# Performance work log

Measured on AMD Instinct MI355X. Metric: run time of the kernel, lower is better.

The kernel has to match this reference:

```python
import jax, jax.numpy as jnp
import numpy as np

B, N, D_NET = 16, 2048, 64
L_SFC, D_VNF = 16, 32
HID, NHEAD, DFF, NLAYERS = 128, 4, 8, 2
NUM_NODES = 1024
SEQ = L_SFC + 2
EPS = 1e-5


def setup_inputs() -> dict:
    key = jax.random.key(0)
    ks = iter(jax.random.split(key, 40))
    def nrm(shape, scale=0.02):
        return (jax.random.normal(next(ks), shape, dtype=jnp.float32) * scale)
    inp = {
        'net_state': jax.random.normal(next(ks), (B, N, D_NET), dtype=jnp.float32),
        'sfc_state': jax.random.normal(next(ks), (B, L_SFC, D_VNF), dtype=jnp.float32),
        'node_pair': jax.random.randint(next(ks), (B, 2), 0, NUM_NODES),
        # manual attention projections (torch Linear layout [out,in])
        'Wq': nrm((4 * D_NET, D_NET)), 'bq': jnp.zeros((4 * D_NET,), jnp.float32),
        'Wk': nrm((4 * D_NET, D_NET)), 'bk': jnp.zeros((4 * D_NET,), jnp.float32),
        'Wv': nrm((4 * D_NET, D_NET)), 'bv': jnp.zeros((4 * D_NET,), jnp.float32),
        'net_W': nrm((HID, 4 * D_NET)), 'net_b': jnp.zeros((HID,), jnp.float32),
        'node_embed': nrm((NUM_NODES, D_VNF), 1.0),
        'sfc_W': nrm((HID, D_VNF)), 'sfc_b': jnp.zeros((HID,), jnp.float32),
        'pos_embed': nrm((SEQ, HID), 1.0),
        # 2 TransformerEncoderLayers, stacked on leading axis
        'qkv_w': nrm((NLAYERS, 3 * HID, HID)), 'qkv_b': jnp.zeros((NLAYERS, 3 * HID), jnp.float32),
        'out_w': nrm((NLAYERS, HID, HID)), 'out_b': jnp.zeros((NLAYERS, HID), jnp.float32),
        'ln1_w': jnp.ones((NLAYERS, HID), jnp.float32), 'ln1_b': jnp.zeros((NLAYERS, HID), jnp.float32),
        'lin1_w': nrm((NLAYERS, DFF, HID)), 'lin1_b': jnp.zeros((NLAYERS, DFF), jnp.float32),
        'lin2_w': nrm((NLAYERS, HID, DFF)), 'lin2_b': jnp.zeros((NLAYERS, HID), jnp.float32),
        'ln2_w': jnp.ones((NLAYERS, HID), jnp.float32), 'ln2_b': jnp.zeros((NLAYERS, HID), jnp.float32),
    }
    return inp


def _layernorm(x, w, b):
    mu = jnp.mean(x, axis=-1, keepdims=True)
    var = jnp.mean(jnp.square(x - mu), axis=-1, keepdims=True)
    return (x - mu) * jax.lax.rsqrt(var + EPS) * w + b


def _mha(x, w_qkv, b_qkv, w_out, b_out, pad_mask):
    Bx, S, H = x.shape
    hd = H // NHEAD
    qkv = x @ w_qkv.T + b_qkv                      # [B,S,3H]
    q, k, v = jnp.split(qkv, 3, axis=-1)
    q = q.reshape(Bx, S, NHEAD, hd).transpose(0, 2, 1, 3)
    k = k.reshape(Bx, S, NHEAD, hd).transpose(0, 2, 1, 3)
    v = v.reshape(Bx, S, NHEAD, hd).transpose(0, 2, 1, 3)
    scores = jnp.einsum('bhqd,bhkd->bhqk', q, k) / jnp.float32(hd) ** 0.5
    scores = scores + jnp.where(pad_mask[:, None, None, :], -1e9, 0.0)
    attn = jax.nn.softmax(scores, axis=-1)
    o = jnp.einsum('bhqk,bhkd->bhqd', attn, v).transpose(0, 2, 1, 3).reshape(Bx, S, H)
    return o @ w_out.T + b_out


def reference(net_state, sfc_state, node_pair, Wq, bq, Wk, bk, Wv, bv,
              net_W, net_b, node_embed, sfc_W, sfc_b, pos_embed,
              qkv_w, qkv_b, out_w, out_b, ln1_w, ln1_b,
              lin1_w, lin1_b, lin2_w, lin2_b, ln2_w, ln2_b):
    # --- net branch: manual single-head self-attention over nodes ---
    Q = net_state @ Wq.T + bq                       # [B,N,4D]
    K = net_state @ Wk.T + bk
    V = net_state @ Wv.T + bv
    scores = jnp.einsum('bnd,bmd->bnm', Q, K) / jnp.float32(net_state.shape[-1]) ** 0.5
    net_out = jax.nn.softmax(scores, axis=-1) @ V   # [B,N,4D]
    net_out = net_out @ net_W.T + net_b             # [B,N,HID]
    # --- sfc branch ---
    pair_emb = node_embed[node_pair]                # [B,2,D_VNF]
    sfc = jnp.concatenate([pair_emb[:, :1], sfc_state, pair_emb[:, 1:2]], axis=1)
    pad_mask = jnp.sum(jnp.abs(sfc), axis=-1) == 0  # [B,SEQ]
    x = sfc @ sfc_W.T + sfc_b + pos_embed[None, :sfc.shape[1]]
    for l in range(NLAYERS):  # post-norm TransformerEncoderLayer, relu, dropout=0
        x = _layernorm(x + _mha(x, qkv_w[l], qkv_b[l], out_w[l], out_b[l], pad_mask), ln1_w[l], ln1_b[l])
        ff = jax.nn.relu(x @ lin1_w[l].T + lin1_b[l]) @ lin2_w[l].T + lin2_b[l]
        x = _layernorm(x + ff, ln2_w[l], ln2_b[l])
    return jnp.concatenate([net_out, x], axis=1)    # [B, N+SEQ, HID]
```

## Files before the change

### kernel.cpp

```cpp
#include <hip/hip_runtime.h>
#include <cstdint>
#include <cstddef>

#define B_   16
#define N_   2048
#define DN   64
#define DQ   256
#define HID_ 128
#define SEQ_ 18
#define OUTR 2066
#define KVB  32

typedef __attribute__((ext_vector_type(4)))  float f32x4;
typedef __attribute__((ext_vector_type(16))) float f32x16;
typedef __attribute__((ext_vector_type(8)))  short bf16x8;

__device__ __forceinline__ unsigned cvtpk(float lo, float hi) {
  unsigned w;
  asm("v_cvt_pk_bf16_f32 %0, %1, %2" : "=v"(w) : "v"(lo), "v"(hi));
  return w;
}
__device__ __forceinline__ short f2bf(float f) {
  union { float f; unsigned u; } v; v.f = f;
  unsigned r = v.u + 0x7fffu + ((v.u >> 16) & 1u);
  return (short)(r >> 16);
}
__device__ __forceinline__ bf16x8 cvt8(const float* p) {
  f32x4 a = *(const f32x4*)p, b = *(const f32x4*)(p + 4);
  union { unsigned u[4]; bf16x8 v; } r;
  r.u[0] = cvtpk(a[0], a[1]); r.u[1] = cvtpk(a[2], a[3]);
  r.u[2] = cvtpk(b[0], b[1]); r.u[3] = cvtpk(b[2], b[3]);
  return r.v;
}
__device__ __forceinline__ float hadd4(f32x4 v) { return (v[0] + v[1]) + (v[2] + v[3]); }

__device__ __forceinline__ bf16x8 mkfrag(unsigned wa, unsigned wb,
                                         unsigned wc, unsigned wd, bool hi) {
  unsigned sa = (unsigned)__shfl_xor((int)wa, 32);
  unsigned sb = (unsigned)__shfl_xor((int)wb, 32);
  unsigned sc = (unsigned)__shfl_xor((int)wc, 32);
  unsigned sd = (unsigned)__shfl_xor((int)wd, 32);
  union { unsigned u[4]; bf16x8 v; } r;
  r.u[0] = hi ? sc : wa;
  r.u[1] = hi ? sd : wb;
  r.u[2] = hi ? wc : sa;
  r.u[3] = hi ? wd : sb;
  return r.v;
}

__global__ __launch_bounds__(512) void proj_kernel(
    const float* __restrict__ net, const float* __restrict__ Wq, const float* __restrict__ bq,
    const float* __restrict__ Wk, const float* __restrict__ bk,
    const float* __restrict__ Wv, const float* __restrict__ bv,
    const float* __restrict__ netW,
    short* __restrict__ Qb, short* __restrict__ Kb, short* __restrict__ Gf) {
  __shared__ char psm[98304];
  short* wl = (short*)psm;
  char* vrm = psm + 32768;

  const int gid = blockIdx.x;
  const int b = gid >> 4;
  const int r0 = (gid & 15) * 128;
  const int t = threadIdx.x;
  const int w = t >> 6, lane = t & 63, ln = lane & 15, g = lane >> 4;
  const int rw = r0 + w * 16;
  const int xk = (ln & 7) << 4;

  bf16x8 af[2];
#pragma unroll
  for (int c = 0; c < 2; ++c)
    af[c] = cvt8(net + ((size_t)b * N_ + rw + ln) * DN + c * 32 + g * 8);

  const float* Ws[3] = {Wq, Wk, Wv};
  for (int m = 0; m < 3; ++m) {
    __syncthreads();
#pragma unroll
    for (int it = 0; it < 8; ++it) {
      int idx = it * 512 + t;
      int row = idx >> 4, c8 = idx & 15;
      f32x4 v = *(const f32x4*)(Ws[m] + row * 64 + c8 * 4);
      int byo = row * 128 + ((c8 * 8) ^ ((row & 7) << 4));
      *(uint2*)((char*)wl + byo) = make_uint2(cvtpk(v[0], v[1]), cvtpk(v[2], v[3]));
    }
    __syncthreads();
    if (m < 2) {
      const float* bias = (m == 0) ? bq : bk;
      short* dst = (m == 0) ? Qb : Kb;
      const float sc = (m == 0) ? 0.125f : 1.0f;
#pragma unroll
      for (int tt = 0; tt < 16; ++tt) {
        f32x4 acc = {0.f, 0.f, 0.f, 0.f};
#pragma unroll
        for (int c = 0; c < 2; ++c) {
          int byo = (tt * 16 + ln) * 128 + ((c * 64 + g * 16) ^ xk);
          bf16x8 wf = *(const bf16x8*)((char*)wl + byo);
          acc = __builtin_amdgcn_mfma_f32_16x16x32_bf16(wf, af[c], acc, 0, 0, 0);
        }
        f32x4 b4 = *(const f32x4*)(bias + tt * 16 + g * 4);
        uint2 u = make_uint2(cvtpk((acc[0] + b4[0]) * sc, (acc[1] + b4[1]) * sc),
                             cvtpk((acc[2] + b4[2]) * sc, (acc[3] + b4[3]) * sc));
        *(uint2*)(dst + ((size_t)b * N_ + rw + ln) * DQ + tt * 16 + g * 4) = u;
      }
    } else {
#pragma unroll
      for (int tt = 0; tt < 16; ++tt) {
        f32x4 acc = {0.f, 0.f, 0.f, 0.f};
#pragma unroll
        for (int c = 0; c < 2; ++c) {
          int byo = (tt * 16 + ln) * 128 + ((c * 64 + g * 16) ^ xk);
          bf16x8 wf = *(const bf16x8*)((char*)wl + byo);
          acc = __builtin_amdgcn_mfma_f32_16x16x32_bf16(af[c], wf, acc, 0, 0, 0);
        }
        float bias = bv[tt * 16 + ln];
        int d = tt * 16 + ln;
#pragma unroll
        for (int r = 0; r < 4; ++r) {
          int nn = w * 16 + g * 4 + r;
          int byte = nn * 512 + ((d * 2) ^ ((nn & 7) << 4));
          *(short*)(vrm + byte) = f2bf(acc[r] + bias);
        }
      }
    }
  }
  __syncthreads();

  const int l31 = lane & 31, h = lane >> 5;
  const bool hb = (h != 0);
#pragma unroll
  for (int j = 0; j < 2; ++j) {
    int ti = w * 2 + j;
    int nt = ti >> 2, dt = ti & 3;
    f32x16 C;
#pragma unroll
    for (int r = 0; r < 16; ++r) C[r] = 0.f;
    int n = nt * 32 + l31;
#pragma unroll
    for (int dc = 0; dc < 16; ++dc) {
      bf16x8 A = *(const bf16x8*)(vrm + n * 512 + ((dc * 32 + h * 16) ^ ((n & 7) << 4)));
      bf16x8 Bf = cvt8(netW + (size_t)(dt * 32 + l31) * DQ + dc * 16 + h * 8);
      C = __builtin_amdgcn_mfma_f32_32x32x16_bf16(A, Bf, C, 0, 0, 0);
    }
    unsigned a0 = cvtpk(C[0],  C[1]),  a1 = cvtpk(C[2],  C[3]);
    unsigned a2 = cvtpk(C[4],  C[5]),  a3 = cvtpk(C[6],  C[7]);
    unsigned a4 = cvtpk(C[8],  C[9]),  a5 = cvtpk(C[10], C[11]);
    unsigned a6 = cvtpk(C[12], C[13]), a7 = cvtpk(C[14], C[15]);
    bf16x8 f0 = mkfrag(a0, a1, a2, a3, hb);
    bf16x8 f1 = mkfrag(a4, a5, a6, a7, hb);
    size_t base = (((size_t)b * 64 + (r0 >> 5) + nt) * 8 + dt * 2) * 512;
    *(bf16x8*)(Gf + base + lane * 8)       = f0;
    *(bf16x8*)(Gf + base + 512 + lane * 8) = f1;
  }
}

struct SfcS {
  float xs[SEQ_][132];
  float qkv[SEQ_][388];
  float scs[4][SEQ_][19];
  float sinb[SEQ_][32];
  float ffh[SEQ_][8];
  float maskv[SEQ_];
  short xbf[32 * 128];
};

__device__ __forceinline__ void par_ln(SfcS& S, const float* __restrict__ lw,
                                       const float* __restrict__ lb, int w, int lane) {
  float w0 = lw[lane * 2], w1 = lw[lane * 2 + 1];
  float b0 = lb[lane * 2], b1 = lb[lane * 2 + 1];
  for (int r = w; r < SEQ_; r += 4) {
    float2 v = *(const float2*)&S.qkv[r][128 + lane * 2];
    float s1 = v.x + v.y;
    float s2 = v.x * v.x + v.y * v.y;
#pragma unroll
    for (int off = 1; off < 64; off <<= 1) {
      s1 += __shfl_xor(s1, off);
      s2 += __shfl_xor(s2, off);
    }
    float mu = s1 * 0.0078125f;
    float var = s2 * 0.0078125f - mu * mu;
    float rsd = rsqrtf(var + 1e-5f);
    S.xs[r][lane * 2]     = (v.x - mu) * rsd * w0 + b0;
    S.xs[r][lane * 2 + 1] = (v.y - mu) * rsd * w1 + b1;
  }
}

__device__ __forceinline__ void rows_to_bf(const float* __restrict__ src, int stride,
                                           char* __restrict__ xbf, int t) {
  for (int i = t; i < SEQ_ * 16; i += 256) {
    int row = i >> 4, c8 = i & 15;
    const float* p = src + row * stride + c8 * 8;
    f32x4 a = *(const f32x4*)p;
    f32x4 b = *(const f32x4*)(p + 4);
    uint4 u;
    u.x = cvtpk(a[0], a[1]); u.y = cvtpk(a[2], a[3]);
    u.z = cvtpk(b[0], b[1]); u.w = cvtpk(b[2], b[3]);
    int byo = row * 256 + ((c8 * 16) ^ ((row & 7) << 4));
    *(uint4*)(xbf + byo) = u;
  }
}

__device__ void sfc_body(
    int b, SfcS& S,
    const float* __restrict__ sfc_state, const int* __restrict__ node_pair,
    const float* __restrict__ node_embed, const float* __restrict__ sfcW,
    const float* __restrict__ sfcb, const float* __restrict__ pos,
    const float* __restrict__ qkvW, const float* __restrict__ qkvB,
    const float* __restrict__ outW, const float* __restrict__ outB,
    const float* __restrict__ ln1w, const float* __restrict__ ln1b,
    const float* __restrict__ l1w, const float* __restrict__ l1b,
    const float* __restrict__ l2w, const float* __restrict__ l2b,
    const float* __restrict__ ln2w, const float* __restrict__ ln2b,
    float* __restrict__ out) {
  const int t = threadIdx.x;
  const int w = t >> 6, lane = t & 63, ln = lane & 15, g = lane >> 4;
  char* xbf = (char*)S.xbf;
  const int xk2 = (ln & 7) << 4;

  for (int i = t; i < 512; i += 256) ((uint4*)xbf)[i] = make_uint4(0, 0, 0, 0);

  for (int i = t; i < SEQ_ * 32; i += 256) {
    int s = i >> 5, d = i & 31;
    float v;
    if (s == 0)       v = node_embed[node_pair[b * 2 + 0] * 32 + d];
    else if (s == 17) v = node_embed[node_pair[b * 2 + 1] * 32 + d];
    else              v = sfc_state[((size_t)b * 16 + (s - 1)) * 32 + d];
    S.sinb[s][d] = v;
  }
  __syncthreads();
  if (t < SEQ_) {
    float sum = 0.f;
#pragma unroll
    for (int d = 0; d < 32; ++d) sum += fabsf(S.sinb[t][d]);
    S.maskv[t] = (sum == 0.f) ? -1e9f : 0.f;
  }
  {
    int hh = t & 127, half = t >> 7;
    f32x4 wr[8];
#pragma unroll
    for (int j = 0; j < 8; ++j) wr[j] = *(const f32x4*)(sfcW + hh * 32 + j * 4);
    for (int si = half * 9; si < half * 9 + 9; ++si) {
      f32x4 a = {0.f, 0.f, 0.f, 0.f};
#pragma unroll
      for (int j = 0; j < 8; ++j) a += wr[j] * (*(const f32x4*)&S.sinb[si][j * 4]);
      S.xs[si][hh] = hadd4(a) + sfcb[hh] + pos[si * HID_ + hh];
    }
  }
  __syncthreads();

  for (int ll = 0; ll < 2; ++ll) {
    rows_to_bf(&S.xs[0][0], 132, xbf, t);
    __syncthreads();
    {
      bf16x8 af[2][4];
#pragma unroll
      for (int m = 0; m < 2; ++m)
#pragma unroll
        for (int k = 0; k < 4; ++k)
          af[m][k] = *(const bf16x8*)(xbf + (m * 16 + ln) * 256 + ((k * 64 + g * 16) ^ xk2));
#pragma unroll
      for (int i = 0; i < 6; ++i) {
        int nt = w + i * 4;
        const float* wp = qkvW + ((size_t)ll * 384 + nt * 16 + ln) * HID_;
        f32x4 a0 = {0.f, 0.f, 0.f, 0.f}, a1 = {0.f, 0.f, 0.f, 0.f};
#pragma unroll
        for (int k = 0; k < 4; ++k) {
          bf16x8 wf = cvt8(wp + k * 32 + g * 8);
          a0 = __builtin_amdgcn_mfma_f32_16x16x32_bf16(wf, af[0][k], a0, 0, 0, 0);
          a1 = __builtin_amdgcn_mfma_f32_16x16x32_bf16(wf, af[1][k], a1, 0, 0, 0);
        }
        f32x4 b4 = *(const f32x4*)(qkvB + ll * 384 + nt * 16 + g * 4);
#pragma unroll
        for (int r = 0; r < 4; ++r) {
          S.qkv[ln][nt * 16 + g * 4 + r] = a0[r] + b4[r];
          if (ln < 2) S.qkv[16 + ln][nt * 16 + g * 4 + r] = a1[r] + b4[r];
        }
      }
    }
    __syncthreads();
    for (int i = t; i < 4 * SEQ_ * SEQ_; i += 256) {
      int hh = i / (SEQ_ * SEQ_), rem = i - hh * SEQ_ * SEQ_;
      int qi = rem / SEQ_, kj = rem - qi * SEQ_;
      f32x4 a = {0.f, 0.f, 0.f, 0.f};
#pragma unroll
      for (int j = 0; j < 8; ++j)
        a += (*(const f32x4*)&S.qkv[qi][hh * 32 + j * 4]) *
             (*(const f32x4*)&S.qkv[kj][128 + hh * 32 + j * 4]);
      S.scs[hh][qi][kj] = hadd4(a) * 0.17677669529663687f + S.maskv[kj];
    }
    __syncthreads();
    if (t < 4 * SEQ_) {
      int hh = t / SEQ_, qi = t - hh * SEQ_;
      float mx = -1e30f;
#pragma unroll
      for (int j = 0; j < SEQ_; ++j) mx = fmaxf(mx, S.scs[hh][qi][j]);
      float sum = 0.f;
#pragma unroll
      for (int j = 0; j < SEQ_; ++j) {
        float e = __expf(S.scs[hh][qi][j] - mx);
        S.scs[hh][qi][j] = e; sum += e;
      }
      float inv = 1.f / sum;
#pragma unroll
      for (int j = 0; j < SEQ_; ++j) S.scs[hh][qi][j] *= inv;
    }
    __syncthreads();
    for (int i = t; i < SEQ_ * HID_; i += 256) {
      int s = i >> 7, hd = i & 127, hh = hd >> 5;
      float a = 0.f;
#pragma unroll
      for (int j = 0; j < SEQ_; ++j) a += S.scs[hh][s][j] * S.qkv[j][256 + hd];
      S.qkv[s][hd] = a;
    }
    __syncthreads();
    rows_to_bf(&S.qkv[0][0], 388, xbf, t);
    __syncthreads();
    {
      bf16x8 af[2][4];
#pragma unroll
      for (int m = 0; m < 2; ++m)
#pragma unroll
        for (int k = 0; k < 4; ++k)
          af[m][k] = *(const bf16x8*)(xbf + (m * 16 + ln) * 256 + ((k * 64 + g * 16) ^ xk2));
#pragma unroll
      for (int i = 0; i < 2; ++i) {
        int nt = w + i * 4;
        const float* wp = outW + ((size_t)ll * HID_ + nt * 16 + ln) * HID_;
        f32x4 a0 = {0.f, 0.f, 0.f, 0.f}, a1 = {0.f, 0.f, 0.f, 0.f};
#pragma unroll
        for (int k = 0; k < 4; ++k) {
          bf16x8 wf = cvt8(wp + k * 32 + g * 8);
          a0 = __builtin_amdgcn_mfma_f32_16x16x32_bf16(wf, af[0][k], a0, 0, 0, 0);
          a1 = __builtin_amdgcn_mfma_f32_16x16x32_bf16(wf, af[1][k], a1, 0, 0, 0);
        }
        f32x4 b4 = *(const f32x4*)(outB + ll * HID_ + nt * 16 + g * 4);
#pragma unroll
        for (int r = 0; r < 4; ++r) {
          int h = nt * 16 + g * 4 + r;
          S.qkv[ln][128 + h] = S.xs[ln][h] + a0[r] + b4[r];
          if (ln < 2) S.qkv[16 + ln][128 + h] = S.xs[16 + ln][h] + a1[r] + b4[r];
        }
      }
    }
    __syncthreads();
    par_ln(S, ln1w + ll * HID_, ln1b + ll * HID_, w, lane);
    __syncthreads();
    if (t < SEQ_ * 8) {
      int s = t >> 3, oo = t & 7;
      const float* wp = l1w + ((size_t)ll * 8 + oo) * HID_;
      f32x4 a = {0.f, 0.f, 0.f, 0.f};
#pragma unroll
      for (int j = 0; j < 32; ++j)
        a += (*(const f32x4*)(wp + j * 4)) * (*(const f32x4*)&S.xs[s][j * 4]);
      S.ffh[s][oo] = fmaxf(hadd4(a) + l1b[ll * 8 + oo], 0.f);
    }
    __syncthreads();
    for (int i = t; i < SEQ_ * HID_; i += 256) {
      int s = i >> 7, h2 = i & 127;
      const float* wp = l2w + ((size_t)ll * HID_ + h2) * 8;
      float a = 0.f;
#pragma unroll
      for (int j = 0; j < 8; ++j) a += wp[j] * S.ffh[s][j];
      S.qkv[s][128 + h2] = S.xs[s][h2] + a + l2b[ll * HID_ + h2];
    }
    __syncthreads();
    par_ln(S, ln2w + ll * HID_, ln2b + ll * HID_, w, lane);
    __syncthreads();
  }
  for (int i = t; i < SEQ_ * HID_; i += 256) {
    int s = i >> 7, h2 = i & 127;
    out[((size_t)b * OUTR + 2048 + s) * HID_ + h2] = S.xs[s][h2];
  }
}

union ASmem { char attn[32768]; SfcS sfc; };

__global__ __launch_bounds__(256, 2) void attn_sfc_kernel(
    const short* __restrict__ Qb, const short* __restrict__ Kb,
    const short* __restrict__ Gf, const float* __restrict__ netb,
    const float* __restrict__ sfc_state, const int* __restrict__ node_pair,
    const float* __restrict__ node_embed, const float* __restrict__ sfcW,
    const float* __restrict__ sfcb, const float* __restrict__ pos,
    const float* __restrict__ qkvW, const float* __restrict__ qkvB,
    const float* __restrict__ outW, const float* __restrict__ outB,
    const float* __restrict__ ln1w, const float* __restrict__ ln1b,
    const float* __restrict__ l1w, const float* __restrict__ l1b,
    const float* __restrict__ l2w, const float* __restrict__ l2b,
    const float* __restrict__ ln2w, const float* __restrict__ ln2b,
    float* __restrict__ out) {
  __shared__ ASmem sm;
  if (blockIdx.x < 16) {
    sfc_body(blockIdx.x, sm.sfc, sfc_state, node_pair, node_embed, sfcW, sfcb, pos,
             qkvW, qkvB, outW, outB, ln1w, ln1b, l1w, l1b, l2w, l2b, ln2w, ln2b, out);
    return;
  }
  const int i = blockIdx.x - 16;
  const int b = (i & 7) * 2 + ((i >> 3) & 1);
  const int q0 = (i >> 4) * 128;
  const int t = threadIdx.x;
  const int w = t >> 6, l = t & 63;
  const int l31 = l & 31, h = l >> 5, l7 = l & 7;
  const int qw = q0 + w * 32;
  const bool hb = (h != 0);

  const short* Kg = Kb + (size_t)b * N_ * DQ;
  char* kb0 = sm.attn;
  char* kb1 = sm.attn + 16384;

  bf16x8 qf[16];
  const short* Qrow = Qb + ((size_t)b * N_ + qw + l31) * DQ + h * 8;
#pragma unroll
  for (int kc = 0; kc < 16; ++kc)
    qf[kc] = *(const bf16x8*)(Qrow + kc * 16);

  f32x16 o[4];
#pragma unroll
  for (int dt = 0; dt < 4; ++dt)
#pragma unroll
    for (int r = 0; r < 16; ++r) o[dt][r] = 0.f;
  float lsum = 0.f;

  auto stage_k = [&](int tile, char* dst) {
#pragma unroll
    for (int it = 0; it < 4; ++it) {
      int idx = w * 4 + it;
      int row = idx * 2 + h;
      int gcol = (l31 * 16) ^ ((row & 7) << 4);
      const char* src = (const char*)(Kg + (size_t)(tile * KVB + row) * DQ) + gcol;
      __builtin_amdgcn_global_load_lds(
          (const __attribute__((address_space(1))) void*)src,
          (__attribute__((address_space(3))) void*)(dst + idx * 1024), 16, 0, 0);
    }
  };

  stage_k(0, kb0);
  __syncthreads();

  const short* Gb = Gf + (size_t)b * 64 * 4096;
  for (int tt = 0; tt < 64; ++tt) {
    char* kc_ = (tt & 1) ? kb1 : kb0;
    if (tt < 63) stage_k(tt + 1, (tt & 1) ? kb0 : kb1);
    const short* gt = Gb + (size_t)tt * 4096 + l * 8;
    bf16x8 vw[8];
#pragma unroll
    for (int f = 0; f < 8; ++f)
      vw[f] = *(const bf16x8*)(gt + f * 512);
    f32x16 s;
#pragma unroll
    for (int r = 0; r < 16; ++r) s[r] = 0.f;
    __builtin_amdgcn_s_setprio(1);
#pragma unroll
    for (int kc = 0; kc < 16; ++kc) {
      bf16x8 kf = *(const bf16x8*)(kc_ + l31 * 512 + ((kc * 32 + h * 16) ^ (l7 << 4)));
      s = __builtin_amdgcn_mfma_f32_32x32x16_bf16(kf, qf[kc], s, 0, 0, 0);
    }
    __builtin_amdgcn_s_setprio(0);
#pragma unroll
    for (int r = 0; r < 16; ++r) { s[r] = __expf(s[r]); lsum += s[r]; }
    unsigned wA = cvtpk(s[0], s[1]),   wB = cvtpk(s[2], s[3]);
    unsigned wC = cvtpk(s[4], s[5]),   wD = cvtpk(s[6], s[7]);
    unsigned wE = cvtpk(s[8], s[9]),   wF = cvtpk(s[10], s[11]);
    unsigned wG = cvtpk(s[12], s[13]), wH = cvtpk(s[14], s[15]);
    bf16x8 pf0 = mkfrag(wA, wB, wC, wD, hb);
    bf16x8 pf1 = mkfrag(wE, wF, wG, wH, hb);
    __builtin_amdgcn_s_setprio(1);
#pragma unroll
    for (int dt = 0; dt < 4; ++dt) {
      o[dt] = __builtin_amdgcn_mfma_f32_32x32x16_bf16(vw[dt * 2],     pf0, o[dt], 0, 0, 0);
      o[dt] = __builtin_amdgcn_mfma_f32_32x32x16_bf16(vw[dt * 2 + 1], pf1, o[dt], 0, 0, 0);
    }
    __builtin_amdgcn_s_setprio(0);
    __syncthreads();
  }

  lsum += __shfl_xor(lsum, 32);
  const float linv = 1.f / lsum;

  float* orow = out + ((size_t)b * OUTR + qw + l31) * HID_;
#pragma unroll
  for (int dt = 0; dt < 4; ++dt) {
#pragma unroll
    for (int rq = 0; rq < 4; ++rq) {
      f32x4 bia = *(const f32x4*)(netb + dt * 32 + rq * 8 + h * 4);
      f32x4 vv;
      vv[0] = o[dt][4 * rq + 0] * linv + bia[0];
      vv[1] = o[dt][4 * rq + 1] * linv + bia[1];
      vv[2] = o[dt][4 * rq + 2] * linv + bia[2];
      vv[3] = o[dt][4 * rq + 3] * linv + bia[3];
      *(f32x4*)(orow + dt * 32 + rq * 8 + h * 4) = vv;
    }
  }
}

extern "C" void kernel_launch(void* const* d_in, const int* in_sizes, int n_in,
                              void* d_out, int out_size, void* d_ws, size_t ws_size,
                              hipStream_t stream) {
  (void)in_sizes; (void)n_in; (void)out_size; (void)ws_size;
  const float* net_state  = (const float*)d_in[0];
  const float* sfc_state  = (const float*)d_in[1];
  const int*   node_pair  = (const int*)d_in[2];
  const float* Wq   = (const float*)d_in[3];
  const float* bq   = (const float*)d_in[4];
  const float* Wk   = (const float*)d_in[5];
  const float* bk   = (const float*)d_in[6];
  const float* Wv   = (const float*)d_in[7];
  const float* bv   = (const float*)d_in[8];
  const float* netW = (const float*)d_in[9];
  const float* netb = (const float*)d_in[10];
  const float* node_embed = (const float*)d_in[11];
  const float* sfcW = (const float*)d_in[12];
  const float* sfcb = (const float*)d_in[13];
  const float* pos  = (const float*)d_in[14];
  const float* qkvW = (const float*)d_in[15];
  const float* qkvB = (const float*)d_in[16];
  const float* outW = (const float*)d_in[17];
  const float* outB = (const float*)d_in[18];
  const float* ln1w = (const float*)d_in[19];
  const float* ln1b = (const float*)d_in[20];
  const float* l1w  = (const float*)d_in[21];
  const float* l1b  = (const float*)d_in[22];
  const float* l2w  = (const float*)d_in[23];
  const float* l2b  = (const float*)d_in[24];
  const float* ln2w = (const float*)d_in[25];
  const float* ln2b = (const float*)d_in[26];
  float* out = (float*)d_out;

  const size_t S = (size_t)B_ * N_ * DQ;
  short* Qb = (short*)d_ws;
  short* Kb = Qb + S;
  short* Gf = Kb + S;

  proj_kernel<<<256, 512, 0, stream>>>(net_state, Wq, bq, Wk, bk, Wv, bv, netW, Qb, Kb, Gf);
  attn_sfc_kernel<<<272, 256, 0, stream>>>(Qb, Kb, Gf, netb,
                                           sfc_state, node_pair, node_embed, sfcW, sfcb, pos,
                                           qkvW, qkvB, outW, outB, ln1w, ln1b, l1w, l1b,
                                           l2w, l2b, ln2w, ln2b, out);
}
```

Measured before the change: 127.0 us.

## Split KV loop across two wave groups per block with LDS reduction

Doubles the attention block to 512 threads. Two groups of four waves each process half of the key sequence with separate double-buffered K staging. Partial outputs and softmax sums are reduced through shared memory before the normalized write. This halves the serial per-block KV loop to expose more parallelism on an under-filled grid, at the cost of more LDS, a reduction step, and idle threads in the sfc path.

```diff
diff --git a/kernel.cpp b/kernel.cpp
--- a/kernel.cpp
+++ b/kernel.cpp
@@ -166,7 +166,7 @@
                                        const float* __restrict__ lb, int w, int lane) {
   float w0 = lw[lane * 2], w1 = lw[lane * 2 + 1];
   float b0 = lb[lane * 2], b1 = lb[lane * 2 + 1];
-  for (int r = w; r < SEQ_; r += 4) {
+  for (int r = w; r < SEQ_; r += 8) {
     float2 v = *(const float2*)&S.qkv[r][128 + lane * 2];
     float s1 = v.x + v.y;
     float s2 = v.x * v.x + v.y * v.y;
@@ -185,7 +185,7 @@
 
 __device__ __forceinline__ void rows_to_bf(const float* __restrict__ src, int stride,
                                            char* __restrict__ xbf, int t) {
-  for (int i = t; i < SEQ_ * 16; i += 256) {
+  for (int i = t; i < SEQ_ * 16; i += 512) {
     int row = i >> 4, c8 = i & 15;
     const float* p = src + row * stride + c8 * 8;
     f32x4 a = *(const f32x4*)p;
@@ -215,9 +215,9 @@
   char* xbf = (char*)S.xbf;
   const int xk2 = (ln & 7) << 4;
 
-  for (int i = t; i < 512; i += 256) ((uint4*)xbf)[i] = make_uint4(0, 0, 0, 0);
-
-  for (int i = t; i < SEQ_ * 32; i += 256) {
+  ((uint4*)xbf)[t] = make_uint4(0, 0, 0, 0);
+
+  for (int i = t; i < SEQ_ * 32; i += 512) {
     int s = i >> 5, d = i & 31;
     float v;
     if (s == 0)       v = node_embed[node_pair[b * 2 + 0] * 32 + d];
@@ -233,11 +233,11 @@
     S.maskv[t] = (sum == 0.f) ? -1e9f : 0.f;
   }
   {
-    int hh = t & 127, half = t >> 7;
+    int hh = t & 127, part = t >> 7;
     f32x4 wr[8];
 #pragma unroll
     for (int j = 0; j < 8; ++j) wr[j] = *(const f32x4*)(sfcW + hh * 32 + j * 4);
-    for (int si = half * 9; si < half * 9 + 9; ++si) {
+    for (int si = part; si < SEQ_; si += 4) {
       f32x4 a = {0.f, 0.f, 0.f, 0.f};
 #pragma unroll
       for (int j = 0; j < 8; ++j) a += wr[j] * (*(const f32x4*)&S.sinb[si][j * 4]);
@@ -249,7 +249,7 @@
   for (int ll = 0; ll < 2; ++ll) {
     rows_to_bf(&S.xs[0][0], 132, xbf, t);
     __syncthreads();
-    {
+    if (t < 256) {
       bf16x8 af[2][4];
 #pragma unroll
       for (int m = 0; m < 2; ++m)
@@ -276,7 +276,7 @@
       }
     }
     __syncthreads();
-    for (int i = t; i < 4 * SEQ_ * SEQ_; i += 256) {
+    for (int i = t; i < 4 * SEQ_ * SEQ_; i += 512) {
       int hh = i / (SEQ_ * SEQ_), rem = i - hh * SEQ_ * SEQ_;
       int qi = rem / SEQ_, kj = rem - qi * SEQ_;
       f32x4 a = {0.f, 0.f, 0.f, 0.f};
@@ -303,7 +303,7 @@
       for (int j = 0; j < SEQ_; ++j) S.scs[hh][qi][j] *= inv;
     }
     __syncthreads();
-    for (int i = t; i < SEQ_ * HID_; i += 256) {
+    for (int i = t; i < SEQ_ * HID_; i += 512) {
       int s = i >> 7, hd = i & 127, hh = hd >> 5;
       float a = 0.f;
 #pragma unroll
@@ -313,7 +313,7 @@
     __syncthreads();
     rows_to_bf(&S.qkv[0][0], 388, xbf, t);
     __syncthreads();
-    {
+    if (t < 256) {
       bf16x8 af[2][4];
 #pragma unroll
       for (int m = 0; m < 2; ++m)
@@ -353,7 +353,7 @@
       S.ffh[s][oo] = fmaxf(hadd4(a) + l1b[ll * 8 + oo], 0.f);
     }
     __syncthreads();
-    for (int i = t; i < SEQ_ * HID_; i += 256) {
+    for (int i = t; i < SEQ_ * HID_; i += 512) {
       int s = i >> 7, h2 = i & 127;
       const float* wp = l2w + ((size_t)ll * HID_ + h2) * 8;
       float a = 0.f;
@@ -365,15 +365,15 @@
     par_ln(S, ln2w + ll * HID_, ln2b + ll * HID_, w, lane);
     __syncthreads();
   }
-  for (int i = t; i < SEQ_ * HID_; i += 256) {
+  for (int i = t; i < SEQ_ * HID_; i += 512) {
     int s = i >> 7, h2 = i & 127;
     out[((size_t)b * OUTR + 2048 + s) * HID_ + h2] = S.xs[s][h2];
   }
 }
 
-union ASmem { char attn[32768]; SfcS sfc; };
-
-__global__ __launch_bounds__(256, 2) void attn_sfc_kernel(
+union ASmem { alignas(16) char attn[66048]; SfcS sfc; };
+
+__global__ __launch_bounds__(512, 2) void attn_sfc_kernel(
     const short* __restrict__ Qb, const short* __restrict__ Kb,
     const short* __restrict__ Gf, const float* __restrict__ netb,
     const float* __restrict__ sfc_state, const int* __restrict__ node_pair,
@@ -397,13 +397,14 @@
   const int q0 = (i >> 4) * 128;
   const int t = threadIdx.x;
   const int w = t >> 6, l = t & 63;
+  const int gr = w >> 2, wq = w & 3;
   const int l31 = l & 31, h = l >> 5, l7 = l & 7;
-  const int qw = q0 + w * 32;
+  const int qw = q0 + wq * 32;
   const bool hb = (h != 0);
 
-  const short* Kg = Kb + (size_t)b * N_ * DQ;
-  char* kb0 = sm.attn;
-  char* kb1 = sm.attn + 16384;
+  const short* Kg = Kb + ((size_t)b * N_ + (size_t)gr * 1024) * DQ;
+  char* kb0 = sm.attn + gr * 32768;
+  char* kb1 = kb0 + 16384;
 
   bf16x8 qf[16];
   const short* Qrow = Qb + ((size_t)b * N_ + qw + l31) * DQ + h * 8;
@@ -421,7 +422,7 @@
   auto stage_k = [&](int tile, char* dst) {
 #pragma unroll
     for (int it = 0; it < 4; ++it) {
-      int idx = w * 4 + it;
+      int idx = wq * 4 + it;
       int row = idx * 2 + h;
       int gcol = (l31 * 16) ^ ((row & 7) << 4);
       const char* src = (const char*)(Kg + (size_t)(tile * KVB + row) * DQ) + gcol;
@@ -435,10 +436,10 @@
   __syncthreads();
 
   const short* Gb = Gf + (size_t)b * 64 * 4096;
-  for (int tt = 0; tt < 64; ++tt) {
+  for (int tt = 0; tt < 32; ++tt) {
     char* kc_ = (tt & 1) ? kb1 : kb0;
-    if (tt < 63) stage_k(tt + 1, (tt & 1) ? kb0 : kb1);
-    const short* gt = Gb + (size_t)tt * 4096 + l * 8;
+    if (tt < 31) stage_k(tt + 1, (tt & 1) ? kb0 : kb1);
+    const short* gt = Gb + (size_t)(gr * 32 + tt) * 4096 + l * 8;
     bf16x8 vw[8];
 #pragma unroll
     for (int f = 0; f < 8; ++f)
@@ -472,20 +473,47 @@
   }
 
   lsum += __shfl_xor(lsum, 32);
-  const float linv = 1.f / lsum;
-
-  float* orow = out + ((size_t)b * OUTR + qw + l31) * HID_;
-#pragma unroll
-  for (int dt = 0; dt < 4; ++dt) {
-#pragma unroll
-    for (int rq = 0; rq < 4; ++rq) {
-      f32x4 bia = *(const f32x4*)(netb + dt * 32 + rq * 8 + h * 4);
-      f32x4 vv;
-      vv[0] = o[dt][4 * rq + 0] * linv + bia[0];
-      vv[1] = o[dt][4 * rq + 1] * linv + bia[1];
-      vv[2] = o[dt][4 * rq + 2] * linv + bia[2];
-      vv[3] = o[dt][4 * rq + 3] * linv + bia[3];
-      *(f32x4*)(orow + dt * 32 + rq * 8 + h * 4) = vv;
+
+  float* lsums = (float*)(sm.attn + 65536);
+  if (w >= 4) {
+    char* base = sm.attn + (w - 4) * 16384;
+#pragma unroll
+    for (int dt = 0; dt < 4; ++dt)
+#pragma unroll
+      for (int rq = 0; rq < 4; ++rq) {
+        f32x4 v;
+        v[0] = o[dt][rq * 4 + 0]; v[1] = o[dt][rq * 4 + 1];
+        v[2] = o[dt][rq * 4 + 2]; v[3] = o[dt][rq * 4 + 3];
+        *(f32x4*)(base + ((dt * 4 + rq) * 64 + l) * 16) = v;
+      }
+    if (l < 32) lsums[(w - 4) * 32 + l31] = lsum;
+  }
+  __syncthreads();
+  if (w < 4) {
+    const char* base = sm.attn + w * 16384;
+#pragma unroll
+    for (int dt = 0; dt < 4; ++dt)
+#pragma unroll
+      for (int rq = 0; rq < 4; ++rq) {
+        f32x4 v = *(const f32x4*)(base + ((dt * 4 + rq) * 64 + l) * 16);
+        o[dt][rq * 4 + 0] += v[0]; o[dt][rq * 4 + 1] += v[1];
+        o[dt][rq * 4 + 2] += v[2]; o[dt][rq * 4 + 3] += v[3];
+      }
+    const float ltot = lsum + lsums[w * 32 + l31];
+    const float linv = 1.f / ltot;
+    float* orow = out + ((size_t)b * OUTR + qw + l31) * HID_;
+#pragma unroll
+    for (int dt = 0; dt < 4; ++dt) {
+#pragma unroll
+      for (int rq = 0; rq < 4; ++rq) {
+        f32x4 bia = *(const f32x4*)(netb + dt * 32 + rq * 8 + h * 4);
+        f32x4 vv;
+        vv[0] = o[dt][4 * rq + 0] * linv + bia[0];
+        vv[1] = o[dt][4 * rq + 1] * linv + bia[1];
+        vv[2] = o[dt][4 * rq + 2] * linv + bia[2];
+        vv[3] = o[dt][4 * rq + 3] * linv + bia[3];
+        *(f32x4*)(orow + dt * 32 + rq * 8 + h * 4) = vv;
+      }
     }
   }
 }
@@ -529,7 +557,7 @@
   short* Gf = Kb + S;
 
   proj_kernel<<<256, 512, 0, stream>>>(net_state, Wq, bq, Wk, bk, Wv, bv, netW, Qb, Kb, Gf);
-  attn_sfc_kernel<<<272, 256, 0, stream>>>(Qb, Kb, Gf, netb,
+  attn_sfc_kernel<<<272, 512, 0, stream>>>(Qb, Kb, Gf, netb,
                                            sfc_state, node_pair, node_embed, sfcW, sfcb, pos,
                                            qkvW, qkvB, outW, outB, ln1w, ln1b, l1w, l1b,
                                            l2w, l2b, ln2w, ln2b, out);
```

After: 143.3 us. 1.13x slower.
